# Performance work log

Hardware: AMD Instinct MI355X
Metric: run time of the kernel (lower is better)

The kernel has to match this reference:

```python
import jax, jax.numpy as jnp
import numpy as np

V, BLK, H, D, L = 32000, 1024, 16, 1024, 3
HD = D // H  # 64
B, T = 4, 1024


def _layernorm(x, g, b, eps=1e-5):
    mu = jnp.mean(x, axis=-1, keepdims=True)
    var = jnp.mean(jnp.square(x - mu), axis=-1, keepdims=True)
    return (x - mu) * jax.lax.rsqrt(var + eps) * g + b


def setup_inputs() -> dict:
    key = jax.random.key(0)
    ks = jax.random.split(key, 32)
    s = 0.02
    inp = {}
    inp["idx"] = jax.random.randint(ks[0], (B, T), 0, V)
    inp["target"] = jax.random.randint(ks[1], (B, T), 0, V)
    inp["tok_emb"] = jax.random.normal(ks[2], (V, D), jnp.float32) * s
    inp["pos_emb"] = jax.random.normal(ks[3], (BLK, D), jnp.float32) * s
    inp["wq"] = jax.random.normal(ks[4], (L, H, D, HD), jnp.float32) * s
    inp["wk"] = jax.random.normal(ks[5], (L, H, D, HD), jnp.float32) * s
    inp["wv"] = jax.random.normal(ks[6], (L, H, D, HD), jnp.float32) * s
    inp["wproj"] = jax.random.normal(ks[7], (L, D, D), jnp.float32) * s
    inp["bproj"] = jnp.zeros((L, D), jnp.float32)
    inp["ln1_g"] = jnp.ones((L, D), jnp.float32)
    inp["ln1_b"] = jnp.zeros((L, D), jnp.float32)
    inp["ln2_g"] = jnp.ones((L, D), jnp.float32)
    inp["ln2_b"] = jnp.zeros((L, D), jnp.float32)
    inp["w1"] = jax.random.normal(ks[8], (L, D, 4 * D), jnp.float32) * s
    inp["b1"] = jnp.zeros((L, 4 * D), jnp.float32)
    inp["w2"] = jax.random.normal(ks[9], (L, 4 * D, D), jnp.float32) * s
    inp["b2"] = jnp.zeros((L, D), jnp.float32)
    inp["lnf_g"] = jnp.ones((D,), jnp.float32)
    inp["lnf_b"] = jnp.zeros((D,), jnp.float32)
    inp["wlm"] = jax.random.normal(ks[10], (D, V), jnp.float32) * s
    inp["blm"] = jnp.zeros((V,), jnp.float32)
    return inp


def reference(idx, target, tok_emb, pos_emb, wq, wk, wv, wproj, bproj,
              ln1_g, ln1_b, ln2_g, ln2_b, w1, b1, w2, b2,
              lnf_g, lnf_b, wlm, blm):
    Bb, Tt = idx.shape
    x = tok_emb[idx] + pos_emb[:Tt]  # [B,T,D]
    mask = jnp.tril(jnp.ones((Tt, Tt), dtype=bool))  # causal
    scale = D ** -0.5  # NOTE: source scales by n_embd**-0.5, not head_size**-0.5
    for l in range(L):
        xn = _layernorm(x, ln1_g[l], ln1_b[l])
        q = jnp.einsum('btd,hde->bhte', xn, wq[l])
        k = jnp.einsum('btd,hde->bhte', xn, wk[l])
        v = jnp.einsum('btd,hde->bhte', xn, wv[l])
        scores = jnp.einsum('bhte,bhse->bhts', q, k) * scale
        scores = jnp.where(mask, scores, -jnp.inf)
        attn = jax.nn.softmax(scores, axis=-1)
        o = jnp.einsum('bhts,bhse->bhte', attn, v)
        o = o.transpose(0, 2, 1, 3).reshape(Bb, Tt, D)  # concat heads
        x = x + o @ wproj[l] + bproj[l]
        xn2 = _layernorm(x, ln2_g[l], ln2_b[l])
        h = jax.nn.relu(xn2 @ w1[l] + b1[l])
        x = x + h @ w2[l] + b2[l]
    x = _layernorm(x, lnf_g, lnf_b)
    logits = x @ wlm + blm  # [B,T,V]
    logp = jax.nn.log_softmax(logits, axis=-1)
    nll = -jnp.take_along_axis(logp, target[..., None], axis=-1)[..., 0]
    loss = jnp.mean(nll)
    return logits, loss
```

## Files before the change

kernel.cpp:

```cpp
#include <hip/hip_runtime.h>
#include <math.h>

#define Dn   1024
#define Hn   16
#define HDn  64
#define Tn   1024
#define Bn   4
#define Vn   32000
#define Ln   3
#define NT   (Bn*Tn)

typedef __attribute__((ext_vector_type(8))) short bf16x8;
typedef __attribute__((ext_vector_type(4))) float f32x4;
typedef __attribute__((ext_vector_type(8))) unsigned short u16x8;

__device__ __forceinline__ float b2f(unsigned short u) {
  union { float f; unsigned int i; } c; c.i = ((unsigned int)u) << 16; return c.f;
}
__device__ __forceinline__ unsigned short f2b(float f) {
  union { float f; unsigned int i; } c; c.f = f;
  unsigned int r = (c.i + 0x7FFFu + ((c.i >> 16) & 1u)) >> 16;
  return (unsigned short)r;
}

#define GLOAD_LDS16(g, l) __builtin_amdgcn_global_load_lds( \
    (const __attribute__((address_space(1))) void*)(g),     \
    (__attribute__((address_space(3))) void*)(l), 16, 0, 0)

__global__ __launch_bounds__(256) void embed_kernel(
    const int* __restrict__ idx, const float* __restrict__ tok,
    const float* __restrict__ pos, float* __restrict__ x) {
  int row = blockIdx.x;
  int t = row & (Tn - 1);
  int token = idx[row];
  const float4* tp = (const float4*)(tok + (size_t)token * Dn);
  const float4* pp = (const float4*)(pos + (size_t)t * Dn);
  float4* xp = (float4*)(x + (size_t)row * Dn);
  int i = threadIdx.x;
  float4 a = tp[i], b = pp[i];
  xp[i] = make_float4(a.x + b.x, a.y + b.y, a.z + b.z, a.w + b.w);
}

__global__ __launch_bounds__(256) void ln_kernel(
    const float* __restrict__ x, const float* __restrict__ g,
    const float* __restrict__ b, unsigned short* __restrict__ y) {
  int row = blockIdx.x;
  const float4* xr = (const float4*)(x + (size_t)row * Dn);
  __shared__ float red[4];
  int lane = threadIdx.x & 63, w = threadIdx.x >> 6;

  float4 v = xr[threadIdx.x];
  float s = v.x + v.y + v.z + v.w;
  #pragma unroll
  for (int o = 32; o > 0; o >>= 1) s += __shfl_down(s, o, 64);
  if (lane == 0) red[w] = s;
  __syncthreads();
  float mu = (red[0] + red[1] + red[2] + red[3]) * (1.0f / Dn);
  __syncthreads();

  float dx = v.x - mu, dy = v.y - mu, dz = v.z - mu, dw = v.w - mu;
  float ss = dx*dx + dy*dy + dz*dz + dw*dw;
  #pragma unroll
  for (int o = 32; o > 0; o >>= 1) ss += __shfl_down(ss, o, 64);
  if (lane == 0) red[w] = ss;
  __syncthreads();
  float var = (red[0] + red[1] + red[2] + red[3]) * (1.0f / Dn);
  float inv = rsqrtf(var + 1e-5f);

  float4 gv = ((const float4*)g)[threadIdx.x];
  float4 bv = ((const float4*)b)[threadIdx.x];
  ushort4 o4;
  o4.x = f2b(dx*inv*gv.x + bv.x);
  o4.y = f2b(dy*inv*gv.y + bv.y);
  o4.z = f2b(dz*inv*gv.z + bv.z);
  o4.w = f2b(dw*inv*gv.w + bv.w);
  ((ushort4*)(y + (size_t)row * Dn))[threadIdx.x] = o4;
}

__global__ __launch_bounds__(256) void wcast_kernel(
    const float* __restrict__ src, unsigned short* __restrict__ dst,
    int K, int M, long long bsk, long long bsh) {
  __shared__ float t[32][33];
  int m0 = blockIdx.x << 5, k0 = blockIdx.y << 5;
  int tid = threadIdx.x;
  int ml = tid & 31, kl = tid >> 5;
  #pragma unroll
  for (int p = 0; p < 4; ++p) {
    int k = k0 + kl + p * 8;
    int m = m0 + ml;
    t[ml][kl + p * 8] = src[(size_t)k * bsk + (size_t)(m >> 6) * bsh + (m & 63)];
  }
  __syncthreads();
  int kl2 = tid & 31, ml2 = tid >> 5;
  #pragma unroll
  for (int p = 0; p < 4; ++p) {
    int m = m0 + ml2 + p * 8;
    int k = k0 + kl2;
    dst[(size_t)m * K + k] = f2b(t[ml2 + p * 8][kl2]);
  }
}

__global__ __launch_bounds__(256) void mm_bf16(
    const unsigned short* __restrict__ A, const unsigned short* __restrict__ BT,
    const float* __restrict__ bias, const float* __restrict__ res,
    float* __restrict__ Cf, unsigned short* __restrict__ Ch,
    int N, int K, int M, int relu) {
  __shared__ __align__(16) unsigned short As[128 * 32];
  __shared__ __align__(16) unsigned short Bs[128 * 32];
  const int tid = threadIdx.x;
  const int lane = tid & 63, w = tid >> 6, g = lane >> 4;
  const int wr = w >> 1, wc = w & 1;
  const int n0 = blockIdx.x << 7, m0 = blockIdx.y << 7;

  f32x4 acc[4][4];
  #pragma unroll
  for (int i = 0; i < 4; ++i)
    #pragma unroll
    for (int j = 0; j < 4; ++j)
      acc[i][j] = (f32x4){0.f, 0.f, 0.f, 0.f};

  const int beta0 = w * 2048 + lane * 16;
  const int beta1 = beta0 + 1024;
  const int r0 = beta0 >> 6, u0 = (beta0 >> 4) & 3;
  const int r1 = beta1 >> 6, u1 = (beta1 >> 4) & 3;
  const int ks0 = u0 ^ ((r0 >> 1) & 3);
  const int ks1 = u1 ^ ((r1 >> 1) & 3);
  const unsigned short* a_g0 = A + (size_t)(n0 + r0) * K + ks0 * 8;
  const unsigned short* a_g1 = A + (size_t)(n0 + r1) * K + ks1 * 8;
  const unsigned short* b_g0 = BT + (size_t)(m0 + r0) * K + ks0 * 8;
  const unsigned short* b_g1 = BT + (size_t)(m0 + r1) * K + ks1 * 8;
  unsigned short* a_l0 = As + w * 1024;
  unsigned short* a_l1 = As + w * 1024 + 512;
  unsigned short* b_l0 = Bs + w * 1024;
  unsigned short* b_l1 = Bs + w * 1024 + 512;

  int a_off[4], b_off[4];
  #pragma unroll
  for (int f = 0; f < 4; ++f) {
    int row = wr * 64 + f * 16 + (lane & 15);
    a_off[f] = row * 64 + ((g ^ ((row >> 1) & 3)) << 4);
    int col = wc * 64 + f * 16 + (lane & 15);
    b_off[f] = col * 64 + ((g ^ ((col >> 1) & 3)) << 4);
  }

  for (int k0 = 0; k0 < K; k0 += 32) {
    __syncthreads();
    GLOAD_LDS16(a_g0 + k0, a_l0);
    GLOAD_LDS16(a_g1 + k0, a_l1);
    GLOAD_LDS16(b_g0 + k0, b_l0);
    GLOAD_LDS16(b_g1 + k0, b_l1);
    __syncthreads();

    bf16x8 af[4], bfr[4];
    #pragma unroll
    for (int f = 0; f < 4; ++f) {
      af[f]  = *(const bf16x8*)((const char*)As + a_off[f]);
      bfr[f] = *(const bf16x8*)((const char*)Bs + b_off[f]);
    }
    #pragma unroll
    for (int i = 0; i < 4; ++i)
      #pragma unroll
      for (int j = 0; j < 4; ++j)
        acc[i][j] = __builtin_amdgcn_mfma_f32_16x16x32_bf16(af[i], bfr[j], acc[i][j], 0, 0, 0);
  }

  #pragma unroll
  for (int fc = 0; fc < 4; ++fc) {
    int colg = m0 + wc * 64 + fc * 16 + (lane & 15);
    float bz = bias ? bias[colg] : 0.f;
    #pragma unroll
    for (int fr = 0; fr < 4; ++fr) {
      #pragma unroll
      for (int i = 0; i < 4; ++i) {
        int rowg = n0 + wr * 64 + fr * 16 + (g << 2) + i;
        float v = acc[fr][fc][i] + bz;
        if (res) v += res[(size_t)rowg * M + colg];
        if (relu) v = fmaxf(v, 0.f);
        if (Cf) Cf[(size_t)rowg * M + colg] = v;
        else    Ch[(size_t)rowg * M + colg] = f2b(v);
      }
    }
  }
}

template<int OMODE>
__global__ __launch_bounds__(512) void mm512_bf16(
    const unsigned short* __restrict__ A, const unsigned short* __restrict__ BT,
    const float* __restrict__ bias, const float* __restrict__ res,
    float* __restrict__ Cf, unsigned short* __restrict__ Ch,
    float* __restrict__ rowsum, int N, int K, int M, int relu) {
  __shared__ __align__(16) unsigned short As[128 * 32];
  __shared__ __align__(16) unsigned short Bs[256 * 32];
  __shared__ float rsum2[OMODE == 4 ? 128 * 4 : 4];
  const int tid = threadIdx.x;
  const int lane = tid & 63, w = tid >> 6, g = lane >> 4;
  const int wr = w >> 2, wc = w & 3;
  const int n0 = blockIdx.x << 7, m0 = blockIdx.y << 8;

  f32x4 acc[4][4];
  #pragma unroll
  for (int i = 0; i < 4; ++i)
    #pragma unroll
    for (int j = 0; j < 4; ++j)
      acc[i][j] = (f32x4){0.f, 0.f, 0.f, 0.f};

  const int arow = tid >> 2, au = tid & 3;
  const int aks = au ^ ((arow >> 1) & 3);
  const unsigned short* a_g = A + (size_t)(n0 + arow) * K + aks * 8;
  unsigned short* a_l = As + tid * 8;
  const int brow0 = tid >> 2,          bu0 = tid & 3;
  const int brow1 = (tid + 512) >> 2,  bu1 = tid & 3;
  const int bks0 = bu0 ^ ((brow0 >> 1) & 3);
  const int bks1 = bu1 ^ ((brow1 >> 1) & 3);
  const unsigned short* b_g0 = BT + (size_t)(m0 + brow0) * K + bks0 * 8;
  const unsigned short* b_g1 = BT + (size_t)(m0 + brow1) * K + bks1 * 8;
  unsigned short* b_l0 = Bs + tid * 8;
  unsigned short* b_l1 = Bs + (tid + 512) * 8;

  int a_off[4], b_off[4];
  #pragma unroll
  for (int f = 0; f < 4; ++f) {
    int row = wr * 64 + f * 16 + (lane & 15);
    a_off[f] = row * 64 + ((g ^ ((row >> 1) & 3)) << 4);
    int col = wc * 64 + f * 16 + (lane & 15);
    b_off[f] = col * 64 + ((g ^ ((col >> 1) & 3)) << 4);
  }

  for (int k0 = 0; k0 < K; k0 += 32) {
    __syncthreads();
    GLOAD_LDS16(a_g + k0, a_l);
    GLOAD_LDS16(b_g0 + k0, b_l0);
    GLOAD_LDS16(b_g1 + k0, b_l1);
    __syncthreads();

    bf16x8 af[4], bfr[4];
    #pragma unroll
    for (int f = 0; f < 4; ++f) {
      af[f]  = *(const bf16x8*)((const char*)As + a_off[f]);
      bfr[f] = *(const bf16x8*)((const char*)Bs + b_off[f]);
    }
    #pragma unroll
    for (int i = 0; i < 4; ++i)
      #pragma unroll
      for (int j = 0; j < 4; ++j)
        acc[i][j] = __builtin_amdgcn_mfma_f32_16x16x32_bf16(af[i], bfr[j], acc[i][j], 0, 0, 0);
  }

  if (OMODE == 0) {
    #pragma unroll
    for (int fc = 0; fc < 4; ++fc) {
      int colg = m0 + wc * 64 + fc * 16 + (lane & 15);
      float bz = bias ? bias[colg] : 0.f;
      #pragma unroll
      for (int fr = 0; fr < 4; ++fr) {
        #pragma unroll
        for (int i = 0; i < 4; ++i) {
          int rowg = n0 + wr * 64 + fr * 16 + (g << 2) + i;
          float v = acc[fr][fc][i] + bz;
          if (res) v += res[(size_t)rowg * M + colg];
          if (relu) v = fmaxf(v, 0.f);
          if (Cf) Cf[(size_t)rowg * M + colg] = v;
          else    Ch[(size_t)rowg * M + colg] = f2b(v);
        }
      }
    }
  } else if (OMODE == 3) {
    unsigned short* kb  = Ch + (size_t)NT * Dn;
    unsigned short* vtb = Ch + 2 * (size_t)NT * Dn;
    #pragma unroll
    for (int fc = 0; fc < 4; ++fc) {
      int colg = m0 + wc * 64 + fc * 16 + (lane & 15);
      int sel = colg >> 10, hh = (colg >> 6) & 15, e = colg & 63;
      #pragma unroll
      for (int fr = 0; fr < 4; ++fr) {
        int rowg0 = n0 + wr * 64 + fr * 16 + (g << 2);
        int b = rowg0 >> 10, t0 = rowg0 & 1023;
        if (sel == 2) {
          ushort4 pk;
          pk.x = f2b(acc[fr][fc][0]); pk.y = f2b(acc[fr][fc][1]);
          pk.z = f2b(acc[fr][fc][2]); pk.w = f2b(acc[fr][fc][3]);
          *(ushort4*)&vtb[(((size_t)(b * 16 + hh) * 64) + e) * 1024 + t0] = pk;
        } else {
          unsigned short* dst = (sel == 0) ? Ch : kb;
          #pragma unroll
          for (int i = 0; i < 4; ++i)
            dst[(((size_t)(b * 16 + hh) * 1024) + t0 + i) * 64 + e] = f2b(acc[fr][fc][i]);
        }
      }
    }
  } else {
    #pragma unroll
    for (int fr = 0; fr < 4; ++fr) {
      #pragma unroll
      for (int i = 0; i < 4; ++i) {
        int rloc = wr * 64 + fr * 16 + (g << 2) + i;
        int rowg = n0 + rloc;
        float es = 0.f;
        #pragma unroll
        for (int fc = 0; fc < 4; ++fc) {
          int colg = m0 + wc * 64 + fc * 16 + (lane & 15);
          float v = acc[fr][fc][i] + bias[colg];
          Cf[(size_t)rowg * M + colg] = v;
          es += __expf(v);
        }
        es += __shfl_xor(es, 1); es += __shfl_xor(es, 2);
        es += __shfl_xor(es, 4); es += __shfl_xor(es, 8);
        if ((lane & 15) == 0) rsum2[rloc * 4 + wc] = es;
      }
    }
    __syncthreads();
    if (tid < 128)
      atomicAdd(&rowsum[n0 + tid],
                rsum2[tid * 4 + 0] + rsum2[tid * 4 + 1] +
                rsum2[tid * 4 + 2] + rsum2[tid * 4 + 3]);
  }
}

__global__ __launch_bounds__(256) void fattn_kernel(
    const unsigned short* __restrict__ qg, const unsigned short* __restrict__ kg,
    const unsigned short* __restrict__ vtg, unsigned short* __restrict__ ob) {
  const int bid = blockIdx.x;
  const int qt = bid & 15, bh = bid >> 4;
  const int b = bh >> 4, h = bh & 15;
  const int tid = threadIdx.x, lane = tid & 63, w = tid >> 6, g = lane >> 4;

  __shared__ __align__(16) unsigned short Ks[64 * 64];
  __shared__ __align__(16) unsigned short Vs[64 * 64];
  __shared__ __align__(16) unsigned short Pb[4][16 * 64];

  const unsigned short* kbase = kg + (size_t)bh * Tn * HDn;
  const unsigned short* vbase = vtg + (size_t)bh * HDn * Tn;

  const int qrow = qt * 64 + w * 16 + (lane & 15);
  const unsigned short* qptr = qg + ((size_t)bh * Tn + qrow) * HDn;
  bf16x8 qf0 = *(const bf16x8*)(qptr + g * 8);
  bf16x8 qf1 = *(const bf16x8*)(qptr + 32 + g * 8);

  f32x4 accO[4];
  #pragma unroll
  for (int dt = 0; dt < 4; ++dt) accO[dt] = (f32x4){0.f, 0.f, 0.f, 0.f};
  float mrun[4] = {-1e30f, -1e30f, -1e30f, -1e30f};
  float lrun[4] = {0.f, 0.f, 0.f, 0.f};

  const float scale = 0.03125f;
  const int qout0 = qt * 64 + w * 16 + 4 * g;

  unsigned short* pb = &Pb[w][0];
  const int nsteps = qt + 1;

  for (int st = 0; st < nsteps; ++st) {
    const int s0 = st * 64;
    __syncthreads();
    #pragma unroll
    for (int r = 0; r < 2; ++r) {
      int c = tid + 256 * r;
      int srow = c >> 3, u = c & 7;
      GLOAD_LDS16(kbase + (size_t)(s0 + srow) * HDn + ((u ^ (srow & 7)) * 8), &Ks[c * 8]);
    }
    #pragma unroll
    for (int r = 0; r < 2; ++r) {
      int c = tid + 256 * r;
      int d = c >> 3, u = c & 7;
      GLOAD_LDS16(vbase + (size_t)d * Tn + s0 + ((u ^ (d & 7)) * 8), &Vs[c * 8]);
    }
    __syncthreads();

    float p[4][4];
    #pragma unroll
    for (int sub = 0; sub < 4; ++sub) {
      int srow = sub * 16 + (lane & 15);
      const char* kr = (const char*)Ks + srow * 128;
      bf16x8 kf0 = *(const bf16x8*)(kr + ((g ^ (srow & 7)) * 16));
      bf16x8 kf1 = *(const bf16x8*)(kr + (((4 + g) ^ (srow & 7)) * 16));
      f32x4 s4 = (f32x4){0.f, 0.f, 0.f, 0.f};
      s4 = __builtin_amdgcn_mfma_f32_16x16x32_bf16(qf0, kf0, s4, 0, 0, 0);
      s4 = __builtin_amdgcn_mfma_f32_16x16x32_bf16(qf1, kf1, s4, 0, 0, 0);
      int sg = s0 + srow;
      #pragma unroll
      for (int i = 0; i < 4; ++i)
        p[sub][i] = (sg > qout0 + i) ? -1e30f : s4[i] * scale;
    }

    #pragma unroll
    for (int i = 0; i < 4; ++i) {
      float v = fmaxf(fmaxf(p[0][i], p[1][i]), fmaxf(p[2][i], p[3][i]));
      v = fmaxf(v, __shfl_xor(v, 1)); v = fmaxf(v, __shfl_xor(v, 2));
      v = fmaxf(v, __shfl_xor(v, 4)); v = fmaxf(v, __shfl_xor(v, 8));
      float nm = fmaxf(mrun[i], v);
      float fac = __expf(mrun[i] - nm);
      mrun[i] = nm;
      #pragma unroll
      for (int dt = 0; dt < 4; ++dt) accO[dt][i] *= fac;
      float sum = 0.f;
      #pragma unroll
      for (int sub = 0; sub < 4; ++sub) {
        float e = __expf(p[sub][i] - nm);
        p[sub][i] = e;
        sum += e;
      }
      sum += __shfl_xor(sum, 1); sum += __shfl_xor(sum, 2);
      sum += __shfl_xor(sum, 4); sum += __shfl_xor(sum, 8);
      lrun[i] = lrun[i] * fac + sum;
    }

    #pragma unroll
    for (int sub = 0; sub < 4; ++sub) {
      int s = sub * 16 + (lane & 15);
      #pragma unroll
      for (int i = 0; i < 4; ++i) {
        int q = 4 * g + i;
        pb[q * 64 + (((s >> 3) ^ (q & 7)) * 8) + (s & 7)] = f2b(p[sub][i]);
      }
    }

    #pragma unroll
    for (int sc = 0; sc < 2; ++sc) {
      int qq = lane & 15;
      bf16x8 pa = *(const bf16x8*)((const char*)pb + qq * 128 + (((sc * 4 + g) ^ (qq & 7)) * 16));
      #pragma unroll
      for (int dt = 0; dt < 4; ++dt) {
        int d = dt * 16 + (lane & 15);
        bf16x8 vf = *(const bf16x8*)((const char*)Vs + d * 128 + (((sc * 4 + g) ^ (d & 7)) * 16));
        accO[dt] = __builtin_amdgcn_mfma_f32_16x16x32_bf16(pa, vf, accO[dt], 0, 0, 0);
      }
    }
  }

  float rinv[4];
  #pragma unroll
  for (int i = 0; i < 4; ++i) rinv[i] = 1.0f / lrun[i];
  #pragma unroll
  for (int dt = 0; dt < 4; ++dt) {
    int dcol = h * 64 + dt * 16 + (lane & 15);
    #pragma unroll
    for (int i = 0; i < 4; ++i) {
      int t = qout0 + i;
      ob[((size_t)(b * Tn + t)) * Dn + dcol] = f2b(accO[dt][i] * rinv[i]);
    }
  }
}

__global__ __launch_bounds__(256) void loss_kernel(
    const float* __restrict__ logits, const float* __restrict__ rowsum,
    const int* __restrict__ target, float* __restrict__ out_loss) {
  __shared__ float red[4];
  int lane = threadIdx.x & 63, w = threadIdx.x >> 6;
  float s = 0.f;
  for (int row = threadIdx.x; row < NT; row += 256) {
    float lt = logits[(size_t)row * Vn + target[row]];
    s += logf(rowsum[row]) - lt;
  }
  #pragma unroll
  for (int off = 32; off > 0; off >>= 1) s += __shfl_down(s, off, 64);
  if (lane == 0) red[w] = s;
  __syncthreads();
  if (threadIdx.x == 0)
    *out_loss = (red[0] + red[1] + red[2] + red[3]) * (1.0f / NT);
}

static inline void launch_wcast(const float* src, unsigned short* dst, int K, int M,
                                long long bsk, long long bsh, hipStream_t s) {
  dim3 g(M >> 5, K >> 5);
  wcast_kernel<<<g, 256, 0, s>>>(src, dst, K, M, bsk, bsh);
}

static inline void launch_mm(const unsigned short* A, const unsigned short* BT,
                             const float* bias, const float* res,
                             float* Cf, unsigned short* Ch,
                             int N, int K, int M, int relu, hipStream_t s) {
  dim3 g(N >> 7, M >> 7);
  mm_bf16<<<g, 256, 0, s>>>(A, BT, bias, res, Cf, Ch, N, K, M, relu);
}

template<int OMODE>
static inline void launch_mm512(const unsigned short* A, const unsigned short* BT,
                                const float* bias, const float* res,
                                float* Cf, unsigned short* Ch, float* rowsum,
                                int N, int K, int M, int relu, hipStream_t s) {
  dim3 g(N >> 7, M >> 8);
  mm512_bf16<OMODE><<<g, 512, 0, s>>>(A, BT, bias, res, Cf, Ch, rowsum, N, K, M, relu);
}

extern "C" void kernel_launch(void* const* d_in, const int* in_sizes, int n_in,
                              void* d_out, int out_size, void* d_ws, size_t ws_size,
                              hipStream_t stream) {
  const int*   idx    = (const int*)d_in[0];
  const int*   target = (const int*)d_in[1];
  const float* tok    = (const float*)d_in[2];
  const float* pos    = (const float*)d_in[3];
  const float* wq     = (const float*)d_in[4];
  const float* wk     = (const float*)d_in[5];
  const float* wv     = (const float*)d_in[6];
  const float* wproj  = (const float*)d_in[7];
  const float* bproj  = (const float*)d_in[8];
  const float* ln1g   = (const float*)d_in[9];
  const float* ln1b   = (const float*)d_in[10];
  const float* ln2g   = (const float*)d_in[11];
  const float* ln2b   = (const float*)d_in[12];
  const float* w1     = (const float*)d_in[13];
  const float* b1     = (const float*)d_in[14];
  const float* w2     = (const float*)d_in[15];
  const float* b2     = (const float*)d_in[16];
  const float* lnfg   = (const float*)d_in[17];
  const float* lnfb   = (const float*)d_in[18];
  const float* wlm    = (const float*)d_in[19];
  const float* blm    = (const float*)d_in[20];

  float* out = (float*)d_out;

  char* p = (char*)d_ws;
  float* x  = (float*)p;                 p += (size_t)NT * Dn * 4;
  unsigned short* xn = (unsigned short*)p; p += (size_t)NT * Dn * 2;
  unsigned short* reg = (unsigned short*)p; p += (size_t)NT * 4 * Dn * 2;
  unsigned short* wT = (unsigned short*)p; p += (size_t)Vn * Dn * 2;
  float* rowsum = (float*)p;

  unsigned short* qb  = reg;
  unsigned short* kb  = reg + (size_t)NT * Dn;
  unsigned short* vtb = reg + 2 * (size_t)NT * Dn;
  unsigned short* ob  = reg + 3 * (size_t)NT * Dn;
  unsigned short* hb  = reg;

  embed_kernel<<<NT, 256, 0, stream>>>(idx, tok, pos, x);

  for (int l = 0; l < Ln; ++l) {
    const float* wq_l = wq + (size_t)l * Hn * Dn * HDn;
    const float* wk_l = wk + (size_t)l * Hn * Dn * HDn;
    const float* wv_l = wv + (size_t)l * Hn * Dn * HDn;

    ln_kernel<<<NT, 256, 0, stream>>>(x, ln1g + l * Dn, ln1b + l * Dn, xn);

    launch_wcast(wq_l, wT,                  Dn, Dn, HDn, (long long)Dn * HDn, stream);
    launch_wcast(wk_l, wT + 1024 * Dn,      Dn, Dn, HDn, (long long)Dn * HDn, stream);
    launch_wcast(wv_l, wT + 2048 * Dn,      Dn, Dn, HDn, (long long)Dn * HDn, stream);
    launch_mm512<3>(xn, wT, nullptr, nullptr, nullptr, qb, nullptr, NT, Dn, 3072, 0, stream);

    fattn_kernel<<<Bn * Hn * (Tn / 64), 256, 0, stream>>>(qb, kb, vtb, ob);

    launch_wcast(wproj + (size_t)l * Dn * Dn, wT, Dn, Dn, Dn, 64, stream);
    launch_mm(ob, wT, bproj + l * Dn, x, x, nullptr, NT, Dn, Dn, 0, stream);

    ln_kernel<<<NT, 256, 0, stream>>>(x, ln2g + l * Dn, ln2b + l * Dn, xn);

    launch_wcast(w1 + (size_t)l * Dn * 4 * Dn, wT, Dn, 4 * Dn, 4 * Dn, 64, stream);
    launch_mm512<0>(xn, wT, b1 + l * 4 * Dn, nullptr, nullptr, hb, nullptr, NT, Dn, 4 * Dn, 1, stream);
    launch_wcast(w2 + (size_t)l * 4 * Dn * Dn, wT, 4 * Dn, Dn, Dn, 64, stream);
    launch_mm(hb, wT, b2 + l * Dn, x, x, nullptr, NT, 4 * Dn, Dn, 0, stream);
  }

  ln_kernel<<<NT, 256, 0, stream>>>(x, lnfg, lnfb, xn);

  hipMemsetAsync(rowsum, 0, NT * sizeof(float), stream);
  launch_wcast(wlm, wT, Dn, Vn, Vn, 64, stream);
  launch_mm512<4>(xn, wT, blm, nullptr, out, nullptr, rowsum, NT, Dn, Vn, 0, stream);

  loss_kernel<<<1, 256, 0, stream>>>(out, rowsum, target, out + (size_t)NT * Vn);
}
```

Before: 1.428 ms.

## Double-buffer LDS tiles in GEMM and flash-attention kernels to overlap loads

Converts the GEMM kernels (mm_bf16, mm512_bf16) and the flash-attention kernel from single-buffered LDS with two syncthreads per step to double-buffered LDS. The next tile is prefetched with global_load_lds while the current one is computed, using explicit vmcnt waits and raw s_barrier. The logits store is also made nontemporal. This is meant to hide global memory latency behind MFMA work, at the cost of twice the LDS per block, which may lower occupancy. It also relies on hand-written waitcnt counts being correct.

```diff
diff --git a/kernel.cpp b/kernel.cpp
--- a/kernel.cpp
+++ b/kernel.cpp
@@ -12,7 +12,6 @@
 
 typedef __attribute__((ext_vector_type(8))) short bf16x8;
 typedef __attribute__((ext_vector_type(4))) float f32x4;
-typedef __attribute__((ext_vector_type(8))) unsigned short u16x8;
 
 __device__ __forceinline__ float b2f(unsigned short u) {
   union { float f; unsigned int i; } c; c.i = ((unsigned int)u) << 16; return c.f;
@@ -26,6 +25,9 @@
 #define GLOAD_LDS16(g, l) __builtin_amdgcn_global_load_lds( \
     (const __attribute__((address_space(1))) void*)(g),     \
     (__attribute__((address_space(3))) void*)(l), 16, 0, 0)
+
+#define SBAR()  __builtin_amdgcn_s_barrier()
+#define SCHED() __builtin_amdgcn_sched_barrier(0)
 
 __global__ __launch_bounds__(256) void embed_kernel(
     const int* __restrict__ idx, const float* __restrict__ tok,
@@ -105,8 +107,8 @@
     const float* __restrict__ bias, const float* __restrict__ res,
     float* __restrict__ Cf, unsigned short* __restrict__ Ch,
     int N, int K, int M, int relu) {
-  __shared__ __align__(16) unsigned short As[128 * 32];
-  __shared__ __align__(16) unsigned short Bs[128 * 32];
+  __shared__ __align__(16) unsigned short As[2][128 * 32];
+  __shared__ __align__(16) unsigned short Bs[2][128 * 32];
   const int tid = threadIdx.x;
   const int lane = tid & 63, w = tid >> 6, g = lane >> 4;
   const int wr = w >> 1, wc = w & 1;
@@ -129,10 +131,6 @@
   const unsigned short* a_g1 = A + (size_t)(n0 + r1) * K + ks1 * 8;
   const unsigned short* b_g0 = BT + (size_t)(m0 + r0) * K + ks0 * 8;
   const unsigned short* b_g1 = BT + (size_t)(m0 + r1) * K + ks1 * 8;
-  unsigned short* a_l0 = As + w * 1024;
-  unsigned short* a_l1 = As + w * 1024 + 512;
-  unsigned short* b_l0 = Bs + w * 1024;
-  unsigned short* b_l1 = Bs + w * 1024 + 512;
 
   int a_off[4], b_off[4];
   #pragma unroll
@@ -143,26 +141,38 @@
     b_off[f] = col * 64 + ((g ^ ((col >> 1) & 3)) << 4);
   }
 
-  for (int k0 = 0; k0 < K; k0 += 32) {
-    __syncthreads();
-    GLOAD_LDS16(a_g0 + k0, a_l0);
-    GLOAD_LDS16(a_g1 + k0, a_l1);
-    GLOAD_LDS16(b_g0 + k0, b_l0);
-    GLOAD_LDS16(b_g1 + k0, b_l1);
-    __syncthreads();
-
-    bf16x8 af[4], bfr[4];
-    #pragma unroll
-    for (int f = 0; f < 4; ++f) {
-      af[f]  = *(const bf16x8*)((const char*)As + a_off[f]);
-      bfr[f] = *(const bf16x8*)((const char*)Bs + b_off[f]);
-    }
-    #pragma unroll
-    for (int i = 0; i < 4; ++i)
-      #pragma unroll
-      for (int j = 0; j < 4; ++j)
-        acc[i][j] = __builtin_amdgcn_mfma_f32_16x16x32_bf16(af[i], bfr[j], acc[i][j], 0, 0, 0);
-  }
+#define MM_STAGE(buf, kk) do {                                   \
+    GLOAD_LDS16(a_g0 + (kk), As[buf] + w * 1024);                \
+    GLOAD_LDS16(a_g1 + (kk), As[buf] + w * 1024 + 512);          \
+    GLOAD_LDS16(b_g0 + (kk), Bs[buf] + w * 1024);                \
+    GLOAD_LDS16(b_g1 + (kk), Bs[buf] + w * 1024 + 512); } while (0)
+
+#define MM_COMPUTE(buf) do {                                     \
+    bf16x8 af[4], bfr[4];                                        \
+    _Pragma("unroll")                                            \
+    for (int f = 0; f < 4; ++f) {                                \
+      af[f]  = *(const bf16x8*)((const char*)As[buf] + a_off[f]);\
+      bfr[f] = *(const bf16x8*)((const char*)Bs[buf] + b_off[f]);\
+    }                                                            \
+    _Pragma("unroll")                                            \
+    for (int i = 0; i < 4; ++i)                                  \
+      _Pragma("unroll")                                          \
+      for (int j = 0; j < 4; ++j)                                \
+        acc[i][j] = __builtin_amdgcn_mfma_f32_16x16x32_bf16(af[i], bfr[j], acc[i][j], 0, 0, 0); } while (0)
+
+  MM_STAGE(0, 0);
+  int cur = 0;
+  for (int k0 = 0; k0 < K - 32; k0 += 32) {
+    MM_STAGE(cur ^ 1, k0 + 32);
+    asm volatile("s_waitcnt vmcnt(4)" ::: "memory");
+    SCHED(); SBAR(); SCHED();
+    MM_COMPUTE(cur);
+    SCHED(); SBAR(); SCHED();
+    cur ^= 1;
+  }
+  asm volatile("s_waitcnt vmcnt(0)" ::: "memory");
+  SCHED(); SBAR(); SCHED();
+  MM_COMPUTE(cur);
 
   #pragma unroll
   for (int fc = 0; fc < 4; ++fc) {
@@ -181,6 +191,8 @@
       }
     }
   }
+#undef MM_STAGE
+#undef MM_COMPUTE
 }
 
 template<int OMODE>
@@ -189,8 +201,8 @@
     const float* __restrict__ bias, const float* __restrict__ res,
     float* __restrict__ Cf, unsigned short* __restrict__ Ch,
     float* __restrict__ rowsum, int N, int K, int M, int relu) {
-  __shared__ __align__(16) unsigned short As[128 * 32];
-  __shared__ __align__(16) unsigned short Bs[256 * 32];
+  __shared__ __align__(16) unsigned short As[2][128 * 32];
+  __shared__ __align__(16) unsigned short Bs[2][256 * 32];
   __shared__ float rsum2[OMODE == 4 ? 128 * 4 : 4];
   const int tid = threadIdx.x;
   const int lane = tid & 63, w = tid >> 6, g = lane >> 4;
@@ -207,15 +219,11 @@
   const int arow = tid >> 2, au = tid & 3;
   const int aks = au ^ ((arow >> 1) & 3);
   const unsigned short* a_g = A + (size_t)(n0 + arow) * K + aks * 8;
-  unsigned short* a_l = As + tid * 8;
-  const int brow0 = tid >> 2,          bu0 = tid & 3;
-  const int brow1 = (tid + 512) >> 2,  bu1 = tid & 3;
-  const int bks0 = bu0 ^ ((brow0 >> 1) & 3);
-  const int bks1 = bu1 ^ ((brow1 >> 1) & 3);
-  const unsigned short* b_g0 = BT + (size_t)(m0 + brow0) * K + bks0 * 8;
+  const int brow1 = (tid + 512) >> 2;
+  const int bks0 = au ^ ((arow >> 1) & 3);
+  const int bks1 = au ^ ((brow1 >> 1) & 3);
+  const unsigned short* b_g0 = BT + (size_t)(m0 + arow) * K + bks0 * 8;
   const unsigned short* b_g1 = BT + (size_t)(m0 + brow1) * K + bks1 * 8;
-  unsigned short* b_l0 = Bs + tid * 8;
-  unsigned short* b_l1 = Bs + (tid + 512) * 8;
 
   int a_off[4], b_off[4];
   #pragma unroll
@@ -226,25 +234,37 @@
     b_off[f] = col * 64 + ((g ^ ((col >> 1) & 3)) << 4);
   }
 
-  for (int k0 = 0; k0 < K; k0 += 32) {
-    __syncthreads();
-    GLOAD_LDS16(a_g + k0, a_l);
-    GLOAD_LDS16(b_g0 + k0, b_l0);
-    GLOAD_LDS16(b_g1 + k0, b_l1);
-    __syncthreads();
-
-    bf16x8 af[4], bfr[4];
-    #pragma unroll
-    for (int f = 0; f < 4; ++f) {
-      af[f]  = *(const bf16x8*)((const char*)As + a_off[f]);
-      bfr[f] = *(const bf16x8*)((const char*)Bs + b_off[f]);
-    }
-    #pragma unroll
-    for (int i = 0; i < 4; ++i)
-      #pragma unroll
-      for (int j = 0; j < 4; ++j)
-        acc[i][j] = __builtin_amdgcn_mfma_f32_16x16x32_bf16(af[i], bfr[j], acc[i][j], 0, 0, 0);
-  }
+#define MM5_STAGE(buf, kk) do {                                  \
+    GLOAD_LDS16(a_g + (kk), As[buf] + tid * 8);                  \
+    GLOAD_LDS16(b_g0 + (kk), Bs[buf] + tid * 8);                 \
+    GLOAD_LDS16(b_g1 + (kk), Bs[buf] + (tid + 512) * 8); } while (0)
+
+#define MM5_COMPUTE(buf) do {                                    \
+    bf16x8 af[4], bfr[4];                                        \
+    _Pragma("unroll")                                            \
+    for (int f = 0; f < 4; ++f) {                                \
+      af[f]  = *(const bf16x8*)((const char*)As[buf] + a_off[f]);\
+      bfr[f] = *(const bf16x8*)((const char*)Bs[buf] + b_off[f]);\
+    }                                                            \
+    _Pragma("unroll")                                            \
+    for (int i = 0; i < 4; ++i)                                  \
+      _Pragma("unroll")                                          \
+      for (int j = 0; j < 4; ++j)                                \
+        acc[i][j] = __builtin_amdgcn_mfma_f32_16x16x32_bf16(af[i], bfr[j], acc[i][j], 0, 0, 0); } while (0)
+
+  MM5_STAGE(0, 0);
+  int cur = 0;
+  for (int k0 = 0; k0 < K - 32; k0 += 32) {
+    MM5_STAGE(cur ^ 1, k0 + 32);
+    asm volatile("s_waitcnt vmcnt(3)" ::: "memory");
+    SCHED(); SBAR(); SCHED();
+    MM5_COMPUTE(cur);
+    SCHED(); SBAR(); SCHED();
+    cur ^= 1;
+  }
+  asm volatile("s_waitcnt vmcnt(0)" ::: "memory");
+  SCHED(); SBAR(); SCHED();
+  MM5_COMPUTE(cur);
 
   if (OMODE == 0) {
     #pragma unroll
@@ -300,7 +320,7 @@
         for (int fc = 0; fc < 4; ++fc) {
           int colg = m0 + wc * 64 + fc * 16 + (lane & 15);
           float v = acc[fr][fc][i] + bias[colg];
-          Cf[(size_t)rowg * M + colg] = v;
+          __builtin_nontemporal_store(v, &Cf[(size_t)rowg * M + colg]);
           es += __expf(v);
         }
         es += __shfl_xor(es, 1); es += __shfl_xor(es, 2);
@@ -314,6 +334,8 @@
                 rsum2[tid * 4 + 0] + rsum2[tid * 4 + 1] +
                 rsum2[tid * 4 + 2] + rsum2[tid * 4 + 3]);
   }
+#undef MM5_STAGE
+#undef MM5_COMPUTE
 }
 
 __global__ __launch_bounds__(256) void fattn_kernel(
@@ -324,8 +346,8 @@
   const int b = bh >> 4, h = bh & 15;
   const int tid = threadIdx.x, lane = tid & 63, w = tid >> 6, g = lane >> 4;
 
-  __shared__ __align__(16) unsigned short Ks[64 * 64];
-  __shared__ __align__(16) unsigned short Vs[64 * 64];
+  __shared__ __align__(16) unsigned short Ks[2][64 * 64];
+  __shared__ __align__(16) unsigned short Vs[2][64 * 64];
   __shared__ __align__(16) unsigned short Pb[4][16 * 64];
 
   const unsigned short* kbase = kg + (size_t)bh * Tn * HDn;
@@ -348,28 +370,38 @@
   unsigned short* pb = &Pb[w][0];
   const int nsteps = qt + 1;
 
+#define FA_STAGE(buf, s0_) do {                                              \
+    _Pragma("unroll")                                                        \
+    for (int r = 0; r < 2; ++r) {                                            \
+      int c = tid + 256 * r;                                                 \
+      int srow = c >> 3, u = c & 7;                                          \
+      GLOAD_LDS16(kbase + (size_t)((s0_) + srow) * HDn + ((u ^ (srow & 7)) * 8), Ks[buf] + c * 8); \
+    }                                                                        \
+    _Pragma("unroll")                                                        \
+    for (int r = 0; r < 2; ++r) {                                            \
+      int c = tid + 256 * r;                                                 \
+      int d = c >> 3, u = c & 7;                                             \
+      GLOAD_LDS16(vbase + (size_t)d * Tn + (s0_) + ((u ^ (d & 7)) * 8), Vs[buf] + c * 8); \
+    } } while (0)
+
+  FA_STAGE(0, 0);
+  int cur = 0;
+
   for (int st = 0; st < nsteps; ++st) {
     const int s0 = st * 64;
-    __syncthreads();
-    #pragma unroll
-    for (int r = 0; r < 2; ++r) {
-      int c = tid + 256 * r;
-      int srow = c >> 3, u = c & 7;
-      GLOAD_LDS16(kbase + (size_t)(s0 + srow) * HDn + ((u ^ (srow & 7)) * 8), &Ks[c * 8]);
-    }
-    #pragma unroll
-    for (int r = 0; r < 2; ++r) {
-      int c = tid + 256 * r;
-      int d = c >> 3, u = c & 7;
-      GLOAD_LDS16(vbase + (size_t)d * Tn + s0 + ((u ^ (d & 7)) * 8), &Vs[c * 8]);
-    }
-    __syncthreads();
+    if (st + 1 < nsteps) {
+      FA_STAGE(cur ^ 1, s0 + 64);
+      asm volatile("s_waitcnt vmcnt(4)" ::: "memory");
+    } else {
+      asm volatile("s_waitcnt vmcnt(0)" ::: "memory");
+    }
+    SCHED(); SBAR(); SCHED();
 
     float p[4][4];
     #pragma unroll
     for (int sub = 0; sub < 4; ++sub) {
       int srow = sub * 16 + (lane & 15);
-      const char* kr = (const char*)Ks + srow * 128;
+      const char* kr = (const char*)Ks[cur] + srow * 128;
       bf16x8 kf0 = *(const bf16x8*)(kr + ((g ^ (srow & 7)) * 16));
       bf16x8 kf1 = *(const bf16x8*)(kr + (((4 + g) ^ (srow & 7)) * 16));
       f32x4 s4 = (f32x4){0.f, 0.f, 0.f, 0.f};
@@ -420,11 +452,15 @@
       #pragma unroll
       for (int dt = 0; dt < 4; ++dt) {
         int d = dt * 16 + (lane & 15);
-        bf16x8 vf = *(const bf16x8*)((const char*)Vs + d * 128 + (((sc * 4 + g) ^ (d & 7)) * 16));
+        bf16x8 vf = *(const bf16x8*)((const char*)Vs[cur] + d * 128 + (((sc * 4 + g) ^ (d & 7)) * 16));
         accO[dt] = __builtin_amdgcn_mfma_f32_16x16x32_bf16(pa, vf, accO[dt], 0, 0, 0);
       }
     }
-  }
+
+    SCHED(); SBAR(); SCHED();
+    cur ^= 1;
+  }
+#undef FA_STAGE
 
   float rinv[4];
   #pragma unroll
```

After: 1.275 ms. 10.8% less time.
